# Kernel tuning notes

Measured on AMD Instinct MI355X. Metric: run time of the kernel, lower is better.

## Reference

```python
import jax, jax.numpy as jnp
import numpy as np
from jax import lax

B, S, H, E, K = 2, 1024, 2048, 16, 4
CAP = int(B * S * 1.5 * K / E)  # capacity = 768
ALPHA = 0.7

def _mlp2(x, w1, b1, w2, b2):
    return jnp.maximum(x @ w1 + b1, 0.0) @ w2 + b2

def setup_inputs() -> dict:
    key = jax.random.key(0)
    ks = iter(jax.random.split(key, 32))
    def w(shape, scale=0.02):
        return (jax.random.normal(next(ks), shape, dtype=jnp.float32) * scale)
    inp = {
        'hidden_states': jax.random.normal(next(ks), (B, S, H), dtype=jnp.float32),
        'mod_image': jax.random.normal(next(ks), (B, S, H), dtype=jnp.float32),
        'mod_genomic': jax.random.normal(next(ks), (B, S, H), dtype=jnp.float32),
        'g_w1': w((H, H)), 'g_b1': jnp.zeros((H,), jnp.float32),
        'g_w2': w((H, E)), 'g_b2': jnp.zeros((E,), jnp.float32),
        'm_w1': w((H, H)), 'm_b1': jnp.zeros((H,), jnp.float32),
        'm_w2': w((H, H)), 'm_b2': jnp.zeros((H,), jnp.float32),
    }
    for p in ('si', 'sg', 'sc', 'sb'):
        inp[p + '_w1'] = w((H, H // 2)); inp[p + '_b1'] = jnp.zeros((H // 2,), jnp.float32)
        inp[p + '_w2'] = w((H // 2, E)); inp[p + '_b2'] = jnp.zeros((E,), jnp.float32)
    return inp

def reference(hidden_states, mod_image, mod_genomic,
              g_w1, g_b1, g_w2, g_b2,
              si_w1, si_b1, si_w2, si_b2,
              sg_w1, sg_b1, sg_w2, sg_b2,
              sc_w1, sc_b1, sc_w2, sc_b2,
              sb_w1, sb_b1, sb_w2, sb_b2,
              m_w1, m_b1, m_w2, m_b2):
    # generalized router probs over experts
    g_probs = jax.nn.softmax(_mlp2(hidden_states, g_w1, g_b1, g_w2, g_b2), axis=-1)
    # missing-modality representation (clinical + biospecimen are missing)
    miss = _mlp2(hidden_states, m_w1, m_b1, m_w2, m_b2)
    # specialized routers: image, genomic (available) + clinical, biospecimen (use miss)
    s_probs = (jax.nn.softmax(_mlp2(mod_image, si_w1, si_b1, si_w2, si_b2), axis=-1)
               + jax.nn.softmax(_mlp2(mod_genomic, sg_w1, sg_b1, sg_w2, sg_b2), axis=-1)
               + jax.nn.softmax(_mlp2(miss, sc_w1, sc_b1, sc_w2, sc_b2), axis=-1)
               + jax.nn.softmax(_mlp2(miss, sb_w1, sb_b1, sb_w2, sb_b2), axis=-1))
    s_probs = s_probs / 2.0  # divided by len(available_modalities) == 2, as in source
    router_probs = ALPHA * g_probs + (1.0 - ALPHA) * s_probs  # [B,S,E]
    top_k_probs, top_k_idx = lax.top_k(router_probs, K)  # [B,S,K]
    top_k_probs = top_k_probs / top_k_probs.sum(axis=-1, keepdims=True)
    onehot = jax.nn.one_hot(top_k_idx, E, dtype=router_probs.dtype)  # [B,S,K,E]
    dmask = onehot.sum(axis=-2)                               # [B,S,E] (0/1: experts distinct)
    cmask = (onehot * top_k_probs[..., None]).sum(axis=-2)    # [B,S,E]
    dispatch = jnp.zeros((B, S, E, CAP), router_probs.dtype).at[..., 0].set(dmask)
    combine = jnp.zeros((B, S, E, CAP), router_probs.dtype).at[..., 0].set(cmask)
    mean_probs = router_probs.mean(axis=(0, 1))  # [E]
    aux_loss = jnp.sum(mean_probs * jnp.log(mean_probs * E + 1e-9))
    return dispatch, combine, router_probs, aux_loss
```

## Files before the change

### kernel.cpp

```cpp
#include <hip/hip_runtime.h>
#include <math.h>
#include <stdint.h>

#define NTOK 2048
#define HDIM 2048
#define HHALF 1024
#define EDIM 16
#define CAPV 768
#define TOPK 4
#define GK 2048

typedef __bf16 bf16x8 __attribute__((ext_vector_type(8)));
typedef __bf16 bf16x4 __attribute__((ext_vector_type(4)));
typedef float f32x4 __attribute__((ext_vector_type(4)));


struct GJobA {
  const __bf16 *Ah, *Al, *Wh, *Wl;
  const float* bias;
  float* Cf; __bf16 *Ch, *Cl;
  int relu, N, blk0;
};
struct GJobsA { GJobA j[6]; };

#define BKA 32
#define NTA 64

#define BARR __builtin_amdgcn_s_barrier()
#define LGKM0 do { asm volatile("s_waitcnt lgkmcnt(0)" ::: "memory"); \
                   __builtin_amdgcn_sched_barrier(0); } while (0)
#define PRIO1 __builtin_amdgcn_s_setprio(1)
#define PRIO0 __builtin_amdgcn_s_setprio(0)

__global__ __launch_bounds__(512, 2) void gemm_phased(GJobsA P) {
  __shared__ __align__(16) __bf16 lds[2][4][256 * BKA];

  const int tid = threadIdx.x;
  const int wid = tid >> 6, lane = tid & 63;
  const int lane15 = lane & 15, c0 = lane >> 4;

  const int bid = blockIdx.x;
  int ji = 0;
#pragma unroll
  for (int k = 1; k < 6; ++k)
    if (bid >= P.j[k].blk0) ji = k;
  const GJobA J = P.j[ji];
  const int local = bid - J.blk0;
  const int nbx = J.N >> 8;
  const int bx = local & (nbx - 1);
  const int by = local / nbx;
  const int m0 = by * 256, n0 = bx * 256;

  const int wr = wid >> 2, wc = wid & 3;

  int srow[2], soff[2];
#pragma unroll
  for (int h = 0; h < 2; ++h) {
    int s = tid + h * 512;
    int row = s >> 2;
    srow[h] = row;
    soff[h] = ((s & 3) ^ ((row >> 1) & 3)) * 8;
  }

  int offB[4], offA[2][4];
#pragma unroll
  for (int ni = 0; ni < 4; ++ni) {
    int rb = wc * 64 + ni * 16 + lane15;
    offB[ni] = rb * 64 + ((c0 ^ ((rb >> 1) & 3)) << 4);
  }
#pragma unroll
  for (int mh = 0; mh < 2; ++mh)
#pragma unroll
    for (int i = 0; i < 4; ++i) {
      int ra = wr * 128 + mh * 64 + i * 16 + lane15;
      offA[mh][i] = ra * 64 + ((c0 ^ ((ra >> 1) & 3)) << 4);
    }

#define STAGE2(gptr, grow0, k1, larr)                                          \
  { _Pragma("unroll") for (int h = 0; h < 2; ++h) {                            \
      const __bf16* _src =                                                     \
          (gptr) + (size_t)((grow0) + srow[h]) * GK + (k1) + soff[h];          \
      __builtin_amdgcn_global_load_lds(                                        \
          (const __attribute__((address_space(1))) uint32_t*)_src,             \
          (__attribute__((address_space(3))) uint32_t*)((larr) +               \
              (wid * 64 + h * 512) * 8), 16, 0, 0); } }

#define DSR_A(dst, base, h)                                                    \
  { _Pragma("unroll") for (int i = 0; i < 4; ++i)                              \
      dst[i] = *(const bf16x8*)((base) + offA[h][i]); }
#define DSR_B(dst, base)                                                       \
  { _Pragma("unroll") for (int i = 0; i < 4; ++i)                              \
      dst[i] = *(const bf16x8*)((base) + offB[i]); }
#define MFMA16(af, bf, mh)                                                     \
  { _Pragma("unroll") for (int mi = 0; mi < 4; ++mi)                           \
    _Pragma("unroll") for (int ni = 0; ni < 4; ++ni)                           \
      acc[(mh) * 4 + mi][ni] = __builtin_amdgcn_mfma_f32_16x16x32_bf16(        \
          af[mi], bf[ni], acc[(mh) * 4 + mi][ni], 0, 0, 0); }

  f32x4 acc[8][4];
#pragma unroll
  for (int i = 0; i < 8; ++i)
#pragma unroll
    for (int j = 0; j < 4; ++j) acc[i][j] = (f32x4){0.f, 0.f, 0.f, 0.f};

  STAGE2(J.Ah, m0, 0, lds[0][0]);
  STAGE2(J.Wh, n0, 0, lds[0][2]);
  STAGE2(J.Wl, n0, 0, lds[0][3]);
  STAGE2(J.Al, m0, 0, lds[0][1]);
  asm volatile("s_waitcnt vmcnt(0)" ::: "memory");
  BARR;

  bf16x8 ah[4], al[4], bh[4], bl[4];

  for (int t = 0; t < NTA; ++t) {
    const int cur = t & 1, nxt = cur ^ 1;
    const bool hasNext = (t + 1 < NTA);
    const int k1 = (t + 1) * BKA;
    const char* cAh = (const char*)lds[cur][0];
    const char* cAl = (const char*)lds[cur][1];
    const char* cBh = (const char*)lds[cur][2];
    const char* cBl = (const char*)lds[cur][3];

    DSR_A(ah, cAh, 0);
    DSR_B(bh, cBh);
    if (hasNext) STAGE2(J.Ah, m0, k1, lds[nxt][0]);
    BARR; LGKM0;
    PRIO1; MFMA16(ah, bh, 0); PRIO0;
    if (hasNext) { asm volatile("s_waitcnt vmcnt(4)" ::: "memory"); }
    else         { asm volatile("s_waitcnt vmcnt(2)" ::: "memory"); }
    BARR;
    DSR_B(bl, cBl);
    if (hasNext) STAGE2(J.Wh, n0, k1, lds[nxt][2]);
    BARR; LGKM0;
    PRIO1; MFMA16(ah, bl, 0); PRIO0;
    if (hasNext) { asm volatile("s_waitcnt vmcnt(4)" ::: "memory"); }
    else         { asm volatile("s_waitcnt vmcnt(0)" ::: "memory"); }
    BARR;
    DSR_A(al, cAl, 0);
    if (hasNext) STAGE2(J.Wl, n0, k1, lds[nxt][3]);
    BARR; LGKM0;
    PRIO1; MFMA16(al, bh, 0); PRIO0;
    BARR;
    DSR_A(ah, cAh, 1);
    if (hasNext) STAGE2(J.Al, m0, k1, lds[nxt][1]);
    BARR; LGKM0;
    PRIO1; MFMA16(ah, bh, 1); PRIO0;
    BARR;
    DSR_A(al, cAl, 1);
    BARR; LGKM0;
    PRIO1; MFMA16(ah, bl, 1); PRIO0;
    BARR;
    PRIO1; MFMA16(al, bh, 1); PRIO0;
    if (hasNext) { asm volatile("s_waitcnt vmcnt(4)" ::: "memory"); }
    BARR;
  }

#pragma unroll
  for (int mh = 0; mh < 2; ++mh)
#pragma unroll
    for (int mi = 0; mi < 4; ++mi)
#pragma unroll
      for (int ni = 0; ni < 4; ++ni) {
        int col = n0 + wc * 64 + ni * 16 + lane15;
        float bv = J.bias[col];
        f32x4 v = acc[mh * 4 + mi][ni];
#pragma unroll
        for (int j = 0; j < 4; ++j) {
          int row = m0 + wr * 128 + mh * 64 + mi * 16 + c0 * 4 + j;
          float x = v[j] + bv;
          if (J.relu) x = fmaxf(x, 0.0f);
          size_t o = (size_t)row * J.N + col;
          if (J.Cf) J.Cf[o] = x;
          if (J.Ch) {
            __bf16 hh = (__bf16)x;
            J.Ch[o] = hh;
            J.Cl[o] = (__bf16)(x - (float)hh);
          }
        }
      }
#undef STAGE2
#undef DSR_A
#undef DSR_B
#undef MFMA16
}

#define BKT 64

struct GJob {
  const __bf16* Ah; const __bf16* Al;
  const __bf16* Wh; const __bf16* Wl;
  const float* bias;
  float* Cf;
  __bf16* Ch; __bf16* Cl;
  int relu; int N; int blk0;
};
struct GJobs { GJob j[4]; int njobs; };

__device__ __forceinline__ void stage_tile(const __bf16* __restrict__ g,
                                           int grow0, int k0,
                                           __bf16* lbase, int wid, int lane) {
  int r_in = lane >> 3;
  int swz_elems = ((lane & 7) ^ r_in) << 3;
#pragma unroll
  for (int i = 0; i < 4; ++i) {
    int row0 = wid * 32 + i * 8;
    const __bf16* src = g + (size_t)(grow0 + row0 + r_in) * GK + k0 + swz_elems;
    __builtin_amdgcn_global_load_lds(
        (const __attribute__((address_space(1))) uint32_t*)src,
        (__attribute__((address_space(3))) uint32_t*)(lbase + row0 * BKT),
        16, 0, 0);
  }
}

__global__ __launch_bounds__(256) void gemm_split(GJobs P) {
  __shared__ __align__(16) __bf16 lds[4 * 128 * BKT];
  __bf16* ldsAh = lds;
  __bf16* ldsAl = lds + 8192;
  __bf16* ldsBh = lds + 16384;
  __bf16* ldsBl = lds + 24576;
  const char* cAh = (const char*)ldsAh;
  const char* cAl = (const char*)ldsAl;
  const char* cBh = (const char*)ldsBh;
  const char* cBl = (const char*)ldsBl;

  const int bid = blockIdx.x;
  int ji = 0;
#pragma unroll
  for (int k = 1; k < 4; ++k)
    if (k < P.njobs && bid >= P.j[k].blk0) ji = k;
  const GJob J = P.j[ji];
  const int local = bid - J.blk0;
  const int nbx = J.N >> 7;
  const int bx = local & (nbx - 1);
  const int by = local / nbx;
  const int m0 = by * 128;
  const int n0 = bx * 128;

  const int tid = threadIdx.x;
  const int wid = tid >> 6;
  const int lane = tid & 63;
  const int lane15 = lane & 15;
  const int c0 = lane >> 4;
  const int wr = wid >> 1;
  const int wc = wid & 1;

  int offA[4][2], offB[4][2];
#pragma unroll
  for (int i = 0; i < 4; ++i) {
    int ra = wr * 64 + i * 16 + lane15;
    int rb = wc * 64 + i * 16 + lane15;
#pragma unroll
    for (int ks = 0; ks < 2; ++ks) {
      offA[i][ks] = ra * 128 + (((ks * 4 + c0) ^ (ra & 7)) << 4);
      offB[i][ks] = rb * 128 + (((ks * 4 + c0) ^ (rb & 7)) << 4);
    }
  }

  f32x4 acc[4][4];
#pragma unroll
  for (int i = 0; i < 4; ++i)
#pragma unroll
    for (int j = 0; j < 4; ++j) acc[i][j] = (f32x4){0.f, 0.f, 0.f, 0.f};

  for (int k0 = 0; k0 < GK; k0 += BKT) {
    stage_tile(J.Ah, m0, k0, ldsAh, wid, lane);
    stage_tile(J.Al, m0, k0, ldsAl, wid, lane);
    stage_tile(J.Wh, n0, k0, ldsBh, wid, lane);
    stage_tile(J.Wl, n0, k0, ldsBl, wid, lane);
    __syncthreads();
#pragma unroll
    for (int ks = 0; ks < 2; ++ks) {
      bf16x8 ah[4], al[4], bh[4], bl[4];
#pragma unroll
      for (int i = 0; i < 4; ++i) {
        ah[i] = *(const bf16x8*)(cAh + offA[i][ks]);
        al[i] = *(const bf16x8*)(cAl + offA[i][ks]);
        bh[i] = *(const bf16x8*)(cBh + offB[i][ks]);
        bl[i] = *(const bf16x8*)(cBl + offB[i][ks]);
      }
#pragma unroll
      for (int mi = 0; mi < 4; ++mi)
#pragma unroll
        for (int ni = 0; ni < 4; ++ni) {
          acc[mi][ni] = __builtin_amdgcn_mfma_f32_16x16x32_bf16(
              ah[mi], bh[ni], acc[mi][ni], 0, 0, 0);
          acc[mi][ni] = __builtin_amdgcn_mfma_f32_16x16x32_bf16(
              ah[mi], bl[ni], acc[mi][ni], 0, 0, 0);
          acc[mi][ni] = __builtin_amdgcn_mfma_f32_16x16x32_bf16(
              al[mi], bh[ni], acc[mi][ni], 0, 0, 0);
        }
    }
    __syncthreads();
  }

#pragma unroll
  for (int mi = 0; mi < 4; ++mi) {
#pragma unroll
    for (int ni = 0; ni < 4; ++ni) {
      int col = n0 + wc * 64 + ni * 16 + lane15;
      float bv = J.bias[col];
      f32x4 v = acc[mi][ni];
#pragma unroll
      for (int j = 0; j < 4; ++j) {
        int row = m0 + wr * 64 + mi * 16 + c0 * 4 + j;
        float x = v[j] + bv;
        if (J.relu) x = fmaxf(x, 0.0f);
        size_t o = (size_t)row * J.N + col;
        if (J.Cf) J.Cf[o] = x;
        if (J.Ch) {
          __bf16 hh = (__bf16)x;
          J.Ch[o] = hh;
          J.Cl[o] = (__bf16)(x - (float)hh);
        }
      }
    }
  }
}

struct SJob { const float* in; __bf16* h; __bf16* l; };
#define SPLIT_BLKS 4096
__global__ __launch_bounds__(256) void split4(SJob a, SJob b, SJob c, SJob d) {
  int job = blockIdx.x >> 12;
  SJob J = (job == 0) ? a : (job == 1) ? b : (job == 2) ? c : d;
  int i = (blockIdx.x & 4095) * 256 + threadIdx.x;
  float4 v = ((const float4*)J.in)[i];
  bf16x4 hv, lv;
  hv.x = (__bf16)v.x; lv.x = (__bf16)(v.x - (float)hv.x);
  hv.y = (__bf16)v.y; lv.y = (__bf16)(v.y - (float)hv.y);
  hv.z = (__bf16)v.z; lv.z = (__bf16)(v.z - (float)hv.z);
  hv.w = (__bf16)v.w; lv.w = (__bf16)(v.w - (float)hv.w);
  ((bf16x4*)J.h)[i] = hv;
  ((bf16x4*)J.l)[i] = lv;
}

struct TJob { const float* W; __bf16* Th; __bf16* Tl; int Nd; };
struct TJobs { TJob j[6]; };
__global__ __launch_bounds__(256) void tsplit(TJobs P) {
  const TJob J = P.j[blockIdx.z];
  int n0 = blockIdx.x * 32;
  if (n0 >= J.Nd) return;
  int k0 = blockIdx.y * 32;
  __shared__ float t[32][33];
  int tx = threadIdx.x & 31, ty = threadIdx.x >> 5;
#pragma unroll
  for (int i = 0; i < 4; ++i) {
    int kk = ty + i * 8;
    t[kk][tx] = J.W[(size_t)(k0 + kk) * J.Nd + n0 + tx];
  }
  __syncthreads();
#pragma unroll
  for (int i = 0; i < 4; ++i) {
    int nn = ty + i * 8;
    float v = t[tx][nn];
    __bf16 hh = (__bf16)v;
    size_t o = (size_t)(n0 + nn) * GK + k0 + tx;
    J.Th[o] = hh;
    J.Tl[o] = (__bf16)(v - (float)hh);
  }
}

__global__ __launch_bounds__(256) void prebias(
    const float* __restrict__ b2,
    const float* __restrict__ W1a, const float* __restrict__ b1a, float* va,
    const float* __restrict__ W1b, const float* __restrict__ b1b, float* vb) {
  const float* W1 = blockIdx.z ? W1b : W1a;
  const float* b1 = blockIdx.z ? b1b : b1a;
  float* v = blockIdx.z ? vb : va;
  int n = blockIdx.x * 256 + threadIdx.x;
  int k0 = blockIdx.y * 256;
  float acc = (blockIdx.y == 0) ? b1[n] : 0.0f;
#pragma unroll 8
  for (int k = 0; k < 256; ++k)
    acc = fmaf(b2[k0 + k], W1[(size_t)(k0 + k) * HHALF + n], acc);
  atomicAdd(&v[n], acc);
}

struct LJob { const float* Y; const float* W2; const float* b2; float* L; int K; };
struct LJobs { LJob j[5]; };
__global__ __launch_bounds__(256) void logits_kernel(LJobs P) {
  const LJob J = P.j[blockIdx.x >> 8];
  const int blk = blockIdx.x & 255;
  const int tid = threadIdx.x;
  const int wid = tid >> 6, lane = tid & 63;
  const int e = lane & 15;
  const int kq = lane >> 4;
  const int tok0 = blk * 8 + wid * 2;
  const float* y0 = J.Y + (size_t)tok0 * J.K;
  const float* y1 = y0 + J.K;
  const int KQ = J.K >> 2;
  const int kbase = kq * KQ;
  float a0 = 0.f, a1 = 0.f;
#pragma unroll 8
  for (int k = 0; k < KQ; ++k) {
    int kk = kbase + k;
    float w = J.W2[(size_t)kk * EDIM + e];
    a0 = fmaf(y0[kk], w, a0);
    a1 = fmaf(y1[kk], w, a1);
  }
  a0 += __shfl_xor(a0, 16); a0 += __shfl_xor(a0, 32);
  a1 += __shfl_xor(a1, 16); a1 += __shfl_xor(a1, 32);
  if (lane < 16) {
    float b = J.b2[e];
    J.L[(size_t)tok0 * EDIM + e] = a0 + b;
    J.L[(size_t)(tok0 + 1) * EDIM + e] = a1 + b;
  }
}

__device__ __forceinline__ void softmax16(const float* __restrict__ L, float* __restrict__ p) {
  float v[16];
  *(float4*)&v[0]  = *(const float4*)&L[0];
  *(float4*)&v[4]  = *(const float4*)&L[4];
  *(float4*)&v[8]  = *(const float4*)&L[8];
  *(float4*)&v[12] = *(const float4*)&L[12];
  float m = v[0];
#pragma unroll
  for (int e = 1; e < 16; ++e) m = fmaxf(m, v[e]);
  float s = 0.0f;
#pragma unroll
  for (int e = 0; e < 16; ++e) { v[e] = expf(v[e] - m); s += v[e]; }
  float inv = 1.0f / s;
#pragma unroll
  for (int e = 0; e < 16; ++e) p[e] = v[e] * inv;
}

__global__ __launch_bounds__(256) void finalize_kernel(
    const float* __restrict__ Lg, const float* __restrict__ Lsi,
    const float* __restrict__ Lsg, const float* __restrict__ Lsc,
    const float* __restrict__ Lsb,
    float* __restrict__ dispatch, float* __restrict__ combine,
    float* __restrict__ router_probs, float* __restrict__ mean_acc) {
  __shared__ float sm[EDIM];
  int tid = threadIdx.x;
  if (tid < EDIM) sm[tid] = 0.0f;
  __syncthreads();

  int tok = blockIdx.x * 256 + tid;
  float pg[16], ps[16], tmp[16], r[16];
  softmax16(Lg + (size_t)tok * EDIM, pg);
  softmax16(Lsi + (size_t)tok * EDIM, ps);
  softmax16(Lsg + (size_t)tok * EDIM, tmp);
#pragma unroll
  for (int e = 0; e < 16; ++e) ps[e] += tmp[e];
  softmax16(Lsc + (size_t)tok * EDIM, tmp);
#pragma unroll
  for (int e = 0; e < 16; ++e) ps[e] += tmp[e];
  softmax16(Lsb + (size_t)tok * EDIM, tmp);
#pragma unroll
  for (int e = 0; e < 16; ++e) ps[e] += tmp[e];

#pragma unroll
  for (int e = 0; e < 16; ++e) {
    float s = ps[e] * 0.5f;
    r[e] = 0.7f * pg[e] + 0.3f * s;
  }

#pragma unroll
  for (int e = 0; e < 16; e += 4) {
    float4 o = {r[e], r[e + 1], r[e + 2], r[e + 3]};
    *(float4*)&router_probs[(size_t)tok * EDIM + e] = o;
  }

#pragma unroll
  for (int e = 0; e < 16; ++e) atomicAdd(&sm[e], r[e]);

  bool used[16];
#pragma unroll
  for (int e = 0; e < 16; ++e) used[e] = false;
  int idx[TOPK];
  float tp[TOPK];
  float tsum = 0.0f;
#pragma unroll
  for (int j = 0; j < TOPK; ++j) {
    float best = -1.0f;
    int bi = 0;
#pragma unroll
    for (int e = 0; e < 16; ++e) {
      bool take = (!used[e]) && (r[e] > best);
      best = take ? r[e] : best;
      bi = take ? e : bi;
    }
    used[bi] = true;
    idx[j] = bi;
    tp[j] = best;
    tsum += best;
  }
  float invt = 1.0f / tsum;
#pragma unroll
  for (int j = 0; j < TOPK; ++j) {
    size_t off = ((size_t)tok * EDIM + idx[j]) * CAPV;
    dispatch[off] = 1.0f;
    combine[off] = tp[j] * invt;
  }

  __syncthreads();
  if (tid < EDIM) atomicAdd(&mean_acc[tid], sm[tid]);
}

__global__ void aux_kernel(const float* __restrict__ mean_acc, float* __restrict__ out_aux) {
  if (threadIdx.x == 0 && blockIdx.x == 0) {
    float s = 0.0f;
    for (int e = 0; e < EDIM; ++e) {
      float m = mean_acc[e] * (1.0f / (float)NTOK);
      s += m * logf(m * (float)EDIM + 1e-9f);
    }
    *out_aux = s;
  }
}

#define MBYTE (1ull << 20)

extern "C" void kernel_launch(void* const* d_in, const int* in_sizes, int n_in,
                              void* d_out, int out_size, void* d_ws, size_t ws_size,
                              hipStream_t stream) {
  const float* X    = (const float*)d_in[0];
  const float* IMG  = (const float*)d_in[1];
  const float* GEN  = (const float*)d_in[2];
  const float* g_w1 = (const float*)d_in[3];
  const float* g_b1 = (const float*)d_in[4];
  const float* g_w2 = (const float*)d_in[5];
  const float* g_b2 = (const float*)d_in[6];
  const float* m_w1 = (const float*)d_in[7];
  const float* m_b1 = (const float*)d_in[8];
  const float* m_w2 = (const float*)d_in[9];
  const float* m_b2 = (const float*)d_in[10];
  const float* si_w1 = (const float*)d_in[11];
  const float* si_b1 = (const float*)d_in[12];
  const float* si_w2 = (const float*)d_in[13];
  const float* si_b2 = (const float*)d_in[14];
  const float* sg_w1 = (const float*)d_in[15];
  const float* sg_b1 = (const float*)d_in[16];
  const float* sg_w2 = (const float*)d_in[17];
  const float* sg_b2 = (const float*)d_in[18];
  const float* sc_w1 = (const float*)d_in[19];
  const float* sc_b1 = (const float*)d_in[20];
  const float* sc_w2 = (const float*)d_in[21];
  const float* sc_b2 = (const float*)d_in[22];
  const float* sb_w1 = (const float*)d_in[23];
  const float* sb_b1 = (const float*)d_in[24];
  const float* sb_w2 = (const float*)d_in[25];
  const float* sb_b2 = (const float*)d_in[26];

  char* wsb = (char*)d_ws;
  __bf16* Xh    = (__bf16*)(wsb + 0 * MBYTE);
  __bf16* Xl    = (__bf16*)(wsb + 8 * MBYTE);
  __bf16* IMGh  = (__bf16*)(wsb + 16 * MBYTE);
  __bf16* IMGl  = (__bf16*)(wsb + 24 * MBYTE);
  __bf16* GENh  = (__bf16*)(wsb + 32 * MBYTE);
  __bf16* GENl  = (__bf16*)(wsb + 40 * MBYTE);
  __bf16* M2h   = (__bf16*)(wsb + 48 * MBYTE);
  __bf16* M2l   = (__bf16*)(wsb + 56 * MBYTE);
  __bf16* Wm1h  = (__bf16*)(wsb + 64 * MBYTE);
  __bf16* Wm1l  = (__bf16*)(wsb + 72 * MBYTE);
  __bf16* Wg1h  = (__bf16*)(wsb + 80 * MBYTE);
  __bf16* Wg1l  = (__bf16*)(wsb + 88 * MBYTE);
  __bf16* Wsch  = (__bf16*)(wsb + 96 * MBYTE);
  __bf16* Wscl  = (__bf16*)(wsb + 100 * MBYTE);
  __bf16* Wsbh  = (__bf16*)(wsb + 104 * MBYTE);
  __bf16* Wsbl  = (__bf16*)(wsb + 108 * MBYTE);
  __bf16* Wsih  = (__bf16*)(wsb + 112 * MBYTE);
  __bf16* Wsil  = (__bf16*)(wsb + 116 * MBYTE);
  __bf16* Wsgh  = (__bf16*)(wsb + 120 * MBYTE);
  __bf16* Wsgl  = (__bf16*)(wsb + 124 * MBYTE);
  __bf16* H1h   = (__bf16*)(wsb + 128 * MBYTE);
  __bf16* H1l   = (__bf16*)(wsb + 136 * MBYTE);
  __bf16* WPsch = (__bf16*)(wsb + 144 * MBYTE);
  __bf16* WPscl = (__bf16*)(wsb + 148 * MBYTE);
  __bf16* WPsbh = (__bf16*)(wsb + 152 * MBYTE);
  __bf16* WPsbl = (__bf16*)(wsb + 156 * MBYTE);
  float*  YG    = (float*)(wsb + 160 * MBYTE);
  float*  YSI   = (float*)(wsb + 176 * MBYTE);
  float*  YSG   = (float*)(wsb + 184 * MBYTE);
  float*  YSC   = (float*)(wsb + 192 * MBYTE);
  float*  YSB   = (float*)(wsb + 200 * MBYTE);
  float* L0 = (float*)(wsb + 208 * MBYTE);
  float* L1 = L0 + NTOK * EDIM;
  float* L2 = L1 + NTOK * EDIM;
  float* L3 = L2 + NTOK * EDIM;
  float* L4 = L3 + NTOK * EDIM;
  float* meanp = L4 + NTOK * EDIM;
  float* zbias = meanp + EDIM;
  float* vsc = zbias + GK;
  float* vsb = vsc + HHALF;

  float* dispatch = (float*)d_out;
  float* combine = dispatch + (size_t)NTOK * EDIM * CAPV;
  float* rp = combine + (size_t)NTOK * EDIM * CAPV;
  float* aux = rp + (size_t)NTOK * EDIM;

  hipMemsetAsync(d_out, 0, (size_t)out_size * sizeof(float), stream);
  hipMemsetAsync(meanp, 0, (EDIM + GK + 2 * HHALF) * sizeof(float), stream);

  dim3 blk(256);

  {
    SJob a{X, Xh, Xl}, b{IMG, IMGh, IMGl}, c{GEN, GENh, GENl}, d{m_w2, M2h, M2l};
    split4<<<4 * SPLIT_BLKS, blk, 0, stream>>>(a, b, c, d);
  }

  {
    TJobs t;
    t.j[0] = {m_w1, Wm1h, Wm1l, HDIM};
    t.j[1] = {g_w1, Wg1h, Wg1l, HDIM};
    t.j[2] = {sc_w1, Wsch, Wscl, HHALF};
    t.j[3] = {sb_w1, Wsbh, Wsbl, HHALF};
    t.j[4] = {si_w1, Wsih, Wsil, HHALF};
    t.j[5] = {sg_w1, Wsgh, Wsgl, HHALF};
    tsplit<<<dim3(64, 64, 6), blk, 0, stream>>>(t);
  }

  prebias<<<dim3(HHALF / 256, 8, 2), blk, 0, stream>>>(m_b2, sc_w1, sc_b1, vsc,
                                                       sb_w1, sb_b1, vsb);

  {
    GJobsA g;
    g.j[0] = {Xh, Xl, Wm1h, Wm1l, m_b1, nullptr, H1h, H1l, 1, HDIM, 0};
    g.j[1] = {Xh, Xl, Wg1h, Wg1l, g_b1, YG, nullptr, nullptr, 1, HDIM, 64};
    g.j[2] = {IMGh, IMGl, Wsih, Wsil, si_b1, YSI, nullptr, nullptr, 1, HHALF, 128};
    g.j[3] = {GENh, GENl, Wsgh, Wsgl, sg_b1, YSG, nullptr, nullptr, 1, HHALF, 160};
    g.j[4] = {Wsch, Wscl, M2h, M2l, zbias, nullptr, WPsch, WPscl, 0, HDIM, 192};
    g.j[5] = {Wsbh, Wsbl, M2h, M2l, zbias, nullptr, WPsbh, WPsbl, 0, HDIM, 224};
    gemm_phased<<<256, dim3(512), 0, stream>>>(g);
  }

  {
    GJobs g;
    g.j[0] = {H1h, H1l, WPsch, WPscl, vsc, YSC, nullptr, nullptr, 1, HHALF, 0};
    g.j[1] = {H1h, H1l, WPsbh, WPsbl, vsb, YSB, nullptr, nullptr, 1, HHALF, 128};
    g.njobs = 2;
    gemm_split<<<256, blk, 0, stream>>>(g);
  }

  {
    LJobs l;
    l.j[0] = {YG, g_w2, g_b2, L0, HDIM};
    l.j[1] = {YSI, si_w2, si_b2, L1, HHALF};
    l.j[2] = {YSG, sg_w2, sg_b2, L2, HHALF};
    l.j[3] = {YSC, sc_w2, sc_b2, L3, HHALF};
    l.j[4] = {YSB, sb_w2, sb_b2, L4, HHALF};
    logits_kernel<<<5 * 256, blk, 0, stream>>>(l);
  }

  finalize_kernel<<<NTOK / 256, blk, 0, stream>>>(L0, L1, L2, L3, L4,
                                                  dispatch, combine, rp, meanp);
  aux_kernel<<<1, 64, 0, stream>>>(meanp, aux);
}
```

Baseline: 421.6 us.

## Merge prep kernels, split-K the second GEMM, restructure phased GEMM pipeline

Three separate ideas. The split, transpose-split and prebias kernels are fused into a single prep launch to cut launch overhead. The second gemm_split is split along K into two halves, which doubles the block count to 512; the partial sums are added and ReLU is applied inside the logits kernel, at the cost of extra fp32 workspace traffic. The phased GEMM main loop is regrouped into fewer barrier phases, issuing more LDS reads and global prefetches per phase with relaxed vmcnt waits, which increases register pressure.

```diff
diff --git a/kernel.cpp b/kernel.cpp
--- a/kernel.cpp
+++ b/kernel.cpp
@@ -107,7 +107,7 @@
   STAGE2(J.Wh, n0, 0, lds[0][2]);
   STAGE2(J.Wl, n0, 0, lds[0][3]);
   STAGE2(J.Al, m0, 0, lds[0][1]);
-  asm volatile("s_waitcnt vmcnt(0)" ::: "memory");
+  asm volatile("s_waitcnt vmcnt(2)" ::: "memory");
   BARR;
 
   bf16x8 ah[4], al[4], bh[4], bl[4];
@@ -123,35 +123,27 @@
 
     DSR_A(ah, cAh, 0);
     DSR_B(bh, cBh);
+    DSR_B(bl, cBl);
     if (hasNext) STAGE2(J.Ah, m0, k1, lds[nxt][0]);
     BARR; LGKM0;
-    PRIO1; MFMA16(ah, bh, 0); PRIO0;
-    if (hasNext) { asm volatile("s_waitcnt vmcnt(4)" ::: "memory"); }
-    else         { asm volatile("s_waitcnt vmcnt(2)" ::: "memory"); }
-    BARR;
-    DSR_B(bl, cBl);
-    if (hasNext) STAGE2(J.Wh, n0, k1, lds[nxt][2]);
-    BARR; LGKM0;
-    PRIO1; MFMA16(ah, bl, 0); PRIO0;
-    if (hasNext) { asm volatile("s_waitcnt vmcnt(4)" ::: "memory"); }
+    PRIO1; MFMA16(ah, bh, 0); MFMA16(ah, bl, 0); PRIO0;
+    if (hasNext) { asm volatile("s_waitcnt vmcnt(2)" ::: "memory"); }
     else         { asm volatile("s_waitcnt vmcnt(0)" ::: "memory"); }
     BARR;
     DSR_A(al, cAl, 0);
-    if (hasNext) STAGE2(J.Wl, n0, k1, lds[nxt][3]);
+    DSR_A(ah, cAh, 1);
+    if (hasNext) {
+      STAGE2(J.Wh, n0, k1, lds[nxt][2]);
+      STAGE2(J.Wl, n0, k1, lds[nxt][3]);
+      STAGE2(J.Al, m0, k1, lds[nxt][1]);
+    }
     BARR; LGKM0;
-    PRIO1; MFMA16(al, bh, 0); PRIO0;
-    BARR;
-    DSR_A(ah, cAh, 1);
-    if (hasNext) STAGE2(J.Al, m0, k1, lds[nxt][1]);
-    BARR; LGKM0;
-    PRIO1; MFMA16(ah, bh, 1); PRIO0;
+    PRIO1; MFMA16(al, bh, 0); MFMA16(ah, bh, 1); PRIO0;
     BARR;
     DSR_A(al, cAl, 1);
     BARR; LGKM0;
-    PRIO1; MFMA16(ah, bl, 1); PRIO0;
-    BARR;
-    PRIO1; MFMA16(al, bh, 1); PRIO0;
-    if (hasNext) { asm volatile("s_waitcnt vmcnt(4)" ::: "memory"); }
+    PRIO1; MFMA16(ah, bl, 1); MFMA16(al, bh, 1); PRIO0;
+    if (hasNext) { asm volatile("s_waitcnt vmcnt(2)" ::: "memory"); }
     BARR;
   }
 
@@ -192,7 +184,7 @@
   const float* bias;
   float* Cf;
   __bf16* Ch; __bf16* Cl;
-  int relu; int N; int blk0;
+  int relu; int N; int blk0; int kLen;
 };
 struct GJobs { GJob j[4]; int njobs; };
 
@@ -262,7 +254,7 @@
 #pragma unroll
     for (int j = 0; j < 4; ++j) acc[i][j] = (f32x4){0.f, 0.f, 0.f, 0.f};
 
-  for (int k0 = 0; k0 < GK; k0 += BKT) {
+  for (int k0 = 0; k0 < J.kLen; k0 += BKT) {
     stage_tile(J.Ah, m0, k0, ldsAh, wid, lane);
     stage_tile(J.Al, m0, k0, ldsAl, wid, lane);
     stage_tile(J.Wh, n0, k0, ldsBh, wid, lane);
@@ -318,64 +310,74 @@
 }
 
 struct SJob { const float* in; __bf16* h; __bf16* l; };
-#define SPLIT_BLKS 4096
-__global__ __launch_bounds__(256) void split4(SJob a, SJob b, SJob c, SJob d) {
-  int job = blockIdx.x >> 12;
-  SJob J = (job == 0) ? a : (job == 1) ? b : (job == 2) ? c : d;
-  int i = (blockIdx.x & 4095) * 256 + threadIdx.x;
-  float4 v = ((const float4*)J.in)[i];
-  bf16x4 hv, lv;
-  hv.x = (__bf16)v.x; lv.x = (__bf16)(v.x - (float)hv.x);
-  hv.y = (__bf16)v.y; lv.y = (__bf16)(v.y - (float)hv.y);
-  hv.z = (__bf16)v.z; lv.z = (__bf16)(v.z - (float)hv.z);
-  hv.w = (__bf16)v.w; lv.w = (__bf16)(v.w - (float)hv.w);
-  ((bf16x4*)J.h)[i] = hv;
-  ((bf16x4*)J.l)[i] = lv;
-}
-
 struct TJob { const float* W; __bf16* Th; __bf16* Tl; int Nd; };
-struct TJobs { TJob j[6]; };
-__global__ __launch_bounds__(256) void tsplit(TJobs P) {
-  const TJob J = P.j[blockIdx.z];
-  int n0 = blockIdx.x * 32;
-  if (n0 >= J.Nd) return;
-  int k0 = blockIdx.y * 32;
-  __shared__ float t[32][33];
-  int tx = threadIdx.x & 31, ty = threadIdx.x >> 5;
-#pragma unroll
-  for (int i = 0; i < 4; ++i) {
-    int kk = ty + i * 8;
-    t[kk][tx] = J.W[(size_t)(k0 + kk) * J.Nd + n0 + tx];
-  }
-  __syncthreads();
-#pragma unroll
-  for (int i = 0; i < 4; ++i) {
-    int nn = ty + i * 8;
-    float v = t[tx][nn];
-    __bf16 hh = (__bf16)v;
-    size_t o = (size_t)(n0 + nn) * GK + k0 + tx;
-    J.Th[o] = hh;
-    J.Tl[o] = (__bf16)(v - (float)hh);
-  }
-}
-
-__global__ __launch_bounds__(256) void prebias(
-    const float* __restrict__ b2,
-    const float* __restrict__ W1a, const float* __restrict__ b1a, float* va,
-    const float* __restrict__ W1b, const float* __restrict__ b1b, float* vb) {
-  const float* W1 = blockIdx.z ? W1b : W1a;
-  const float* b1 = blockIdx.z ? b1b : b1a;
-  float* v = blockIdx.z ? vb : va;
-  int n = blockIdx.x * 256 + threadIdx.x;
-  int k0 = blockIdx.y * 256;
-  float acc = (blockIdx.y == 0) ? b1[n] : 0.0f;
+struct PrepArgs {
+  SJob s[4];
+  TJob t[6];
+  const float* pb2;
+  const float* pW1a; const float* pb1a; float* pva;
+  const float* pW1b; const float* pb1b; float* pvb;
+};
+
+__global__ __launch_bounds__(256) void prep(PrepArgs P) {
+  __shared__ float tbuf[32][33];
+  const int bid = blockIdx.x;
+  const int tid = threadIdx.x;
+  if (bid < 16384) {
+    SJob J = P.s[bid >> 12];
+    int i = (bid & 4095) * 256 + tid;
+    float4 v = ((const float4*)J.in)[i];
+    bf16x4 hv, lv;
+    hv.x = (__bf16)v.x; lv.x = (__bf16)(v.x - (float)hv.x);
+    hv.y = (__bf16)v.y; lv.y = (__bf16)(v.y - (float)hv.y);
+    hv.z = (__bf16)v.z; lv.z = (__bf16)(v.z - (float)hv.z);
+    hv.w = (__bf16)v.w; lv.w = (__bf16)(v.w - (float)hv.w);
+    ((bf16x4*)J.h)[i] = hv;
+    ((bf16x4*)J.l)[i] = lv;
+  } else if (bid < 32768) {
+    int local = bid - 16384;
+    int ji, ln;
+    if (local < 4096)      { ji = 0; ln = local; }
+    else if (local < 8192) { ji = 1; ln = local - 4096; }
+    else { ji = 2 + ((local - 8192) >> 11); ln = (local - 8192) & 2047; }
+    TJob J = P.t[ji];
+    int full = (J.Nd == HDIM);
+    int n0 = (full ? (ln & 63) : (ln & 31)) * 32;
+    int k0 = (full ? (ln >> 6) : (ln >> 5)) * 32;
+    int tx = tid & 31, ty = tid >> 5;
+#pragma unroll
+    for (int i = 0; i < 4; ++i) {
+      int kk = ty + i * 8;
+      tbuf[kk][tx] = J.W[(size_t)(k0 + kk) * J.Nd + n0 + tx];
+    }
+    __syncthreads();
+#pragma unroll
+    for (int i = 0; i < 4; ++i) {
+      int nn = ty + i * 8;
+      float v = tbuf[tx][nn];
+      __bf16 hh = (__bf16)v;
+      size_t o = (size_t)(n0 + nn) * GK + k0 + tx;
+      J.Th[o] = hh;
+      J.Tl[o] = (__bf16)(v - (float)hh);
+    }
+  } else {
+    int local = bid - 32768;
+    int side = local >> 5; int r = local & 31;
+    const float* W1 = side ? P.pW1b : P.pW1a;
+    const float* b1 = side ? P.pb1b : P.pb1a;
+    float* v = side ? P.pvb : P.pva;
+    int n = (r & 3) * 256 + tid;
+    int k0 = (r >> 2) * 256;
+    float acc = (k0 == 0) ? b1[n] : 0.0f;
 #pragma unroll 8
-  for (int k = 0; k < 256; ++k)
-    acc = fmaf(b2[k0 + k], W1[(size_t)(k0 + k) * HHALF + n], acc);
-  atomicAdd(&v[n], acc);
-}
-
-struct LJob { const float* Y; const float* W2; const float* b2; float* L; int K; };
+    for (int k = 0; k < 256; ++k)
+      acc = fmaf(P.pb2[k0 + k], W1[(size_t)(k0 + k) * HHALF + n], acc);
+    atomicAdd(&v[n], acc);
+  }
+}
+
+struct LJob { const float* Y; const float* Y2; const float* W2;
+              const float* b2; float* L; int K; int relu; };
 struct LJobs { LJob j[5]; };
 __global__ __launch_bounds__(256) void logits_kernel(LJobs P) {
   const LJob J = P.j[blockIdx.x >> 8];
@@ -387,15 +389,29 @@
   const int tok0 = blk * 8 + wid * 2;
   const float* y0 = J.Y + (size_t)tok0 * J.K;
   const float* y1 = y0 + J.K;
+  const float* z0 = J.Y2 + (size_t)tok0 * J.K;
+  const float* z1 = z0 + J.K;
   const int KQ = J.K >> 2;
   const int kbase = kq * KQ;
   float a0 = 0.f, a1 = 0.f;
+  if (J.relu) {
 #pragma unroll 8
-  for (int k = 0; k < KQ; ++k) {
-    int kk = kbase + k;
-    float w = J.W2[(size_t)kk * EDIM + e];
-    a0 = fmaf(y0[kk], w, a0);
-    a1 = fmaf(y1[kk], w, a1);
+    for (int k = 0; k < KQ; ++k) {
+      int kk = kbase + k;
+      float w = J.W2[(size_t)kk * EDIM + e];
+      float v0 = fmaxf(y0[kk] + z0[kk], 0.0f);
+      float v1 = fmaxf(y1[kk] + z1[kk], 0.0f);
+      a0 = fmaf(v0, w, a0);
+      a1 = fmaf(v1, w, a1);
+    }
+  } else {
+#pragma unroll 8
+    for (int k = 0; k < KQ; ++k) {
+      int kk = kbase + k;
+      float w = J.W2[(size_t)kk * EDIM + e];
+      a0 = fmaf(y0[kk], w, a0);
+      a1 = fmaf(y1[kk], w, a1);
+    }
   }
   a0 += __shfl_xor(a0, 16); a0 += __shfl_xor(a0, 32);
   a1 += __shfl_xor(a1, 16); a1 += __shfl_xor(a1, 32);
@@ -570,9 +586,11 @@
   float*  YG    = (float*)(wsb + 160 * MBYTE);
   float*  YSI   = (float*)(wsb + 176 * MBYTE);
   float*  YSG   = (float*)(wsb + 184 * MBYTE);
-  float*  YSC   = (float*)(wsb + 192 * MBYTE);
-  float*  YSB   = (float*)(wsb + 200 * MBYTE);
-  float* L0 = (float*)(wsb + 208 * MBYTE);
+  float*  YSCp0 = (float*)(wsb + 192 * MBYTE);
+  float*  YSCp1 = (float*)(wsb + 200 * MBYTE);
+  float*  YSBp0 = (float*)(wsb + 208 * MBYTE);
+  float*  YSBp1 = (float*)(wsb + 216 * MBYTE);
+  float* L0 = (float*)(wsb + 224 * MBYTE);
   float* L1 = L0 + NTOK * EDIM;
   float* L2 = L1 + NTOK * EDIM;
   float* L3 = L2 + NTOK * EDIM;
@@ -593,23 +611,22 @@
   dim3 blk(256);
 
   {
-    SJob a{X, Xh, Xl}, b{IMG, IMGh, IMGl}, c{GEN, GENh, GENl}, d{m_w2, M2h, M2l};
-    split4<<<4 * SPLIT_BLKS, blk, 0, stream>>>(a, b, c, d);
-  }
-
-  {
-    TJobs t;
-    t.j[0] = {m_w1, Wm1h, Wm1l, HDIM};
-    t.j[1] = {g_w1, Wg1h, Wg1l, HDIM};
-    t.j[2] = {sc_w1, Wsch, Wscl, HHALF};
-    t.j[3] = {sb_w1, Wsbh, Wsbl, HHALF};
-    t.j[4] = {si_w1, Wsih, Wsil, HHALF};
-    t.j[5] = {sg_w1, Wsgh, Wsgl, HHALF};
-    tsplit<<<dim3(64, 64, 6), blk, 0, stream>>>(t);
-  }
-
-  prebias<<<dim3(HHALF / 256, 8, 2), blk, 0, stream>>>(m_b2, sc_w1, sc_b1, vsc,
-                                                       sb_w1, sb_b1, vsb);
+    PrepArgs p;
+    p.s[0] = {X, Xh, Xl};
+    p.s[1] = {IMG, IMGh, IMGl};
+    p.s[2] = {GEN, GENh, GENl};
+    p.s[3] = {m_w2, M2h, M2l};
+    p.t[0] = {m_w1, Wm1h, Wm1l, HDIM};
+    p.t[1] = {g_w1, Wg1h, Wg1l, HDIM};
+    p.t[2] = {sc_w1, Wsch, Wscl, HHALF};
+    p.t[3] = {sb_w1, Wsbh, Wsbl, HHALF};
+    p.t[4] = {si_w1, Wsih, Wsil, HHALF};
+    p.t[5] = {sg_w1, Wsgh, Wsgl, HHALF};
+    p.pb2 = m_b2;
+    p.pW1a = sc_w1; p.pb1a = sc_b1; p.pva = vsc;
+    p.pW1b = sb_w1; p.pb1b = sb_b1; p.pvb = vsb;
+    prep<<<32832, blk, 0, stream>>>(p);
+  }
 
   {
     GJobsA g;
@@ -624,19 +641,23 @@
 
   {
     GJobs g;
-    g.j[0] = {H1h, H1l, WPsch, WPscl, vsc, YSC, nullptr, nullptr, 1, HHALF, 0};
-    g.j[1] = {H1h, H1l, WPsbh, WPsbl, vsb, YSB, nullptr, nullptr, 1, HHALF, 128};
-    g.njobs = 2;
-    gemm_split<<<256, blk, 0, stream>>>(g);
+    g.j[0] = {H1h, H1l, WPsch, WPscl, vsc, YSCp0, nullptr, nullptr, 0, HHALF, 0, 1024};
+    g.j[1] = {H1h + 1024, H1l + 1024, WPsch + 1024, WPscl + 1024, zbias, YSCp1,
+              nullptr, nullptr, 0, HHALF, 128, 1024};
+    g.j[2] = {H1h, H1l, WPsbh, WPsbl, vsb, YSBp0, nullptr, nullptr, 0, HHALF, 256, 1024};
+    g.j[3] = {H1h + 1024, H1l + 1024, WPsbh + 1024, WPsbl + 1024, zbias, YSBp1,
+              nullptr, nullptr, 0, HHALF, 384, 1024};
+    g.njobs = 4;
+    gemm_split<<<512, blk, 0, stream>>>(g);
   }
 
   {
     LJobs l;
-    l.j[0] = {YG, g_w2, g_b2, L0, HDIM};
-    l.j[1] = {YSI, si_w2, si_b2, L1, HHALF};
-    l.j[2] = {YSG, sg_w2, sg_b2, L2, HHALF};
-    l.j[3] = {YSC, sc_w2, sc_b2, L3, HHALF};
-    l.j[4] = {YSB, sb_w2, sb_b2, L4, HHALF};
+    l.j[0] = {YG, YG, g_w2, g_b2, L0, HDIM, 0};
+    l.j[1] = {YSI, YSI, si_w2, si_b2, L1, HHALF, 0};
+    l.j[2] = {YSG, YSG, sg_w2, sg_b2, L2, HHALF, 0};
+    l.j[3] = {YSCp0, YSCp1, sc_w2, sc_b2, L3, HHALF, 1};
+    l.j[4] = {YSBp0, YSBp1, sb_w2, sb_b2, L4, HHALF, 1};
     logits_kernel<<<5 * 256, blk, 0, stream>>>(l);
   }
 
```

Result: faster. 405.8 us (-3.8%).
